# Performance work log

Measured on AMD Instinct MI355X. Metric: run time of the kernel, lower is better.

The kernel has to match this reference:

```python
import jax, jax.numpy as jnp
import numpy as np

N = 500000
EMB = 256
CONT = {0: [0, 1, 4, 6, 7, 8, 9, 10, 11, 12, 13],
        1: [0, 1, 4, 5, 6, 7, 8, 9, 10, 11, 12, 13],
        2: [1, 2, 4, 5, 6, 7, 8, 9, 10, 11, 12, 13],
        3: [2, 3, 4, 5, 6, 7, 8, 9, 10, 11, 12, 13]}
DISC = {0: [2, 3, 5], 1: [2, 3], 2: [0], 3: [0, 1]}
DIMS = {0: {2: 96, 3: 8, 5: 2}, 1: {2: 4, 3: 22}, 2: {0: 6}, 3: {0: 15, 1: 96}}


def _splits(n):
    # emb_dim split across n discrete features, remainder to the first ones
    per, r = EMB // n, EMB % n
    return [per + (1 if i < r else 0) for i in range(n)]


def setup_inputs() -> dict:
    key = jax.random.key(0)
    x = jax.random.normal(jax.random.fold_in(key, 0), (N, 14), jnp.float32)
    # discrete columns must hold valid integer codes for every node type using them
    col_max = {0: 6, 1: 96, 2: 4, 3: 8, 5: 2}
    for c, m in col_max.items():
        v = jax.random.randint(jax.random.fold_in(key, 100 + c), (N,), 0, m)
        x = x.at[:, c].set(v.astype(jnp.float32))
    node_types = jax.random.randint(jax.random.fold_in(key, 1), (N,), 0, 4)
    inp = {"x": x, "node_types": node_types}
    for t in range(4):
        fan_in = len(CONT[t])
        s = float(np.sqrt(6.0 / (fan_in + EMB)))  # xavier_uniform bound
        inp[f"W{t}"] = jax.random.uniform(jax.random.fold_in(key, 10 + t), (EMB, fan_in), jnp.float32, -s, s)
        inp[f"b{t}"] = jax.random.uniform(jax.random.fold_in(key, 20 + t), (EMB,), jnp.float32, -0.05, 0.05)
        dims = _splits(len(DISC[t]))
        for i, c in enumerate(DISC[t]):
            vocab = DIMS[t][c]
            se = float(np.sqrt(6.0 / (vocab + dims[i])))
            inp[f"E{t}_{c}"] = jax.random.uniform(jax.random.fold_in(key, 1000 + 10 * t + c), (vocab, dims[i]), jnp.float32, -se, se)
    return inp


def _forward(x, node_types, Ws, bs, Es):
    out = jnp.zeros((x.shape[0], EMB), x.dtype)
    for t in range(4):  # fixed small set of node types (static MoE dispatch)
        mask = node_types == t  # [N]
        # discrete embeddings: gather per feature column, concat to [N, EMB]
        disc = jnp.concatenate(
            [Es[t][i][x[:, c].astype(jnp.int32)] for i, c in enumerate(DISC[t])], axis=1)
        # continuous projection: [N, in_dim] @ [in_dim, EMB] + bias
        cont = x[:, jnp.array(CONT[t])] @ Ws[t].T + bs[t]
        out = jnp.where(mask[:, None], disc + cont, out)
    return out


def reference(x, node_types, W0, b0, W1, b1, W2, b2, W3, b3,
              E0_2, E0_3, E0_5, E1_2, E1_3, E2_0, E3_0, E3_1):
    Ws = [W0, W1, W2, W3]
    bs = [b0, b1, b2, b3]
    Es = {0: [E0_2, E0_3, E0_5], 1: [E1_2, E1_3], 2: [E2_0], 3: [E3_0, E3_1]}
    return _forward(x, node_types, Ws, bs, Es)
```

## Files before the change

### kernel.cpp

```cpp
#include <hip/hip_runtime.h>

typedef float fvec4 __attribute__((ext_vector_type(4)));

#define NBLK 256
#define TPB  1024
#define NG   16
#define CN   512

#define LAUNDER_PTR(p) asm volatile("" : "+v"(p))

#define O_E0_2 0
#define O_E0_3 8450
#define O_E0_5 9155
#define O_E1_2 9332
#define O_E1_3 9844
#define O_E2_0 12660
#define O_E3_0 14196
#define O_E3_1 16116
#define NTAB   28404
#define XSH    NTAB
#define IDX    (XSH + CN * 16)
#define CNTO   (IDX + 4 * CN)
#define SMEM_FLOATS (CNTO + 4)
#define SMEM_BYTES  (SMEM_FLOATS * 4)

extern __shared__ float smem[];

#define FMA4(K, XV)                                   \
    acc.x = fmaf(w[0][K], (XV), acc.x);               \
    acc.y = fmaf(w[1][K], (XV), acc.y);               \
    acc.z = fmaf(w[2][K], (XV), acc.z);               \
    acc.w = fmaf(w[3][K], (XV), acc.w);

__global__ __launch_bounds__(TPB, 1)
void node_enc_kernel(const float* __restrict__ x,
                     const int* __restrict__ node_types,
                     const float* __restrict__ W0, const float* __restrict__ b0,
                     const float* __restrict__ E0_2, const float* __restrict__ E0_3,
                     const float* __restrict__ E0_5,
                     const float* __restrict__ W1, const float* __restrict__ b1,
                     const float* __restrict__ E1_2, const float* __restrict__ E1_3,
                     const float* __restrict__ W2, const float* __restrict__ b2,
                     const float* __restrict__ E2_0,
                     const float* __restrict__ W3, const float* __restrict__ b3,
                     const float* __restrict__ E3_0, const float* __restrict__ E3_1,
                     float* __restrict__ out, int n_nodes)
{
    const int tid = threadIdx.x;
    const int q   = tid & 63;
    const int h   = tid >> 6;

    auto copy_tab = [&](const float* __restrict__ src, int dst, int n) {
        if ((((uintptr_t)src) & 15) == 0) {
            const int nv = n >> 2;
            for (int i = tid; i < nv; i += TPB) {
                const fvec4 v = *(reinterpret_cast<const fvec4*>(src) + i);
                *reinterpret_cast<fvec4*>(&smem[dst + (i << 2)]) = v;
            }
            for (int i = (nv << 2) + tid; i < n; i += TPB) smem[dst + i] = src[i];
        } else {
            for (int i = tid; i < n; i += TPB) smem[dst + i] = src[i];
        }
    };
    auto copy_tab_pad = [&](const float* __restrict__ src, int dst, int rows, int cols) {
        const int n = rows * cols;
        for (int i = tid; i < n; i += TPB) {
            const int r = i / cols, c2 = i - r * cols;
            smem[dst + r * 88 + c2] = src[i];
        }
    };
    copy_tab_pad(E0_2, O_E0_2, 96, 86);
    copy_tab_pad(E0_3, O_E0_3, 8, 85);
    copy_tab_pad(E0_5, O_E0_5, 2, 85);
    copy_tab(E1_2, O_E1_2, 512);
    copy_tab(E1_3, O_E1_3, 2816);
    copy_tab(E2_0, O_E2_0, 1536);
    copy_tab(E3_0, O_E3_0, 1920);
    copy_tab(E3_1, O_E3_1, 12288);

    const int nch = (n_nodes + CN - 1) / CN;
    const int c0  = (int)(((long long)blockIdx.x * nch) / NBLK);
    const int c1  = (int)(((long long)(blockIdx.x + 1) * nch) / NBLK);

    int* const idx_m = reinterpret_cast<int*>(&smem[IDX]);
    int* const cnt_m = reinterpret_cast<int*>(&smem[CNTO]);
    const int* idx_ro = idx_m;
    const int* cnt_ro = cnt_m;

    auto stage_issue = [&](int c, fvec4& r0, fvec4& r1,
                           float& rs, int& ty, int& nv, int& total, int& cnn) {
        const long long cb = (long long)c * CN;
        cnn   = min(CN, (int)(n_nodes - cb));
        total = cnn * 14;
        nv    = total >> 2;
        const fvec4* vsrc = reinterpret_cast<const fvec4*>(x + cb * 14);
        if (tid < nv)          r0 = __builtin_nontemporal_load(vsrc + tid);
        if (tid + TPB < nv)    r1 = __builtin_nontemporal_load(vsrc + tid + TPB);
        const int sf = (nv << 2) + tid;
        if (sf < total) rs = x[cb * 14 + sf];
        if (tid < cnn)  ty = node_types[cb + tid];
    };
    auto stage_write = [&](const fvec4& r0, const fvec4& r1,
                           float rs, int nv, int total) {
        auto wr1 = [&](int i, const fvec4& v) {
            const int f = i << 2;
            int node = f / 14, col = f - node * 14;
            #pragma unroll
            for (int j = 0; j < 4; ++j) {
                smem[XSH + node * 16 + col] = v[j];
                if (++col == 14) { col = 0; ++node; }
            }
        };
        if (tid < nv)        wr1(tid, r0);
        if (tid + TPB < nv)  wr1(tid + TPB, r1);
        const int sf = (nv << 2) + tid;
        if (sf < total) { const int node = sf / 14, col = sf - node * 14; smem[XSH + node * 16 + col] = rs; }
    };

    auto do_chunk = [&](int c) {
        const long long cb = (long long)c * CN;

        {
            const int m = cnt_ro[0];
            const float* Wp = W0; LAUNDER_PTR(Wp);
            const float* bp = b0; LAUNDER_PTR(bp);
            float w[4][11];
            #pragma unroll
            for (int j = 0; j < 4; ++j) {
                #pragma unroll
                for (int k = 0; k < 11; ++k) w[j][k] = Wp[(4 * q + j) * 11 + k];
            }
            float4 bias;
            bias.x = bp[4 * q]; bias.y = bp[4 * q + 1];
            bias.z = bp[4 * q + 2]; bias.w = bp[4 * q + 3];
            int scv, ebase;
            const bool fb = (q == 21) || (q == 42);
            if (q <= 21)      { scv = 2; ebase = O_E0_2 + 4 * q; }
            else if (q <= 42) { scv = 3; ebase = (O_E0_3 - 86) + 4 * q; }
            else              { scv = 5; ebase = (O_E0_5 - 171) + 4 * q; }
            for (int g = h; g < m; g += NG) {
                const int nl = idx_ro[0 * CN + g];
                const float* xr = &smem[XSH + nl * 16];
                const float4 ra = *reinterpret_cast<const float4*>(xr);
                const float4 rb = *reinterpret_cast<const float4*>(xr + 4);
                const float4 rc = *reinterpret_cast<const float4*>(xr + 8);
                const float2 rd = *reinterpret_cast<const float2*>(xr + 12);
                float4 acc = bias;
                FMA4(0,  ra.x) FMA4(1,  ra.y) FMA4(2,  rb.x) FMA4(3,  rb.z)
                FMA4(4,  rb.w) FMA4(5,  rc.x) FMA4(6,  rc.y) FMA4(7,  rc.z)
                FMA4(8,  rc.w) FMA4(9,  rd.x) FMA4(10, rd.y)
                float4 ev;
                if (fb) {
                    if (q == 21) {
                        const int c2 = (int)xr[2], c3 = (int)xr[3];
                        ev.x = smem[O_E0_2 + c2 * 88 + 84];
                        ev.y = smem[O_E0_2 + c2 * 88 + 85];
                        ev.z = smem[O_E0_3 + c3 * 88 + 0];
                        ev.w = smem[O_E0_3 + c3 * 88 + 1];
                    } else {
                        const int c3 = (int)xr[3], c5 = (int)xr[5];
                        ev.x = smem[O_E0_3 + c3 * 88 + 82];
                        ev.y = smem[O_E0_3 + c3 * 88 + 83];
                        ev.z = smem[O_E0_3 + c3 * 88 + 84];
                        ev.w = smem[O_E0_5 + c5 * 88 + 0];
                    }
                } else {
                    const int code = (int)xr[scv];
                    ev = *reinterpret_cast<const float4*>(&smem[ebase + code * 88]);
                }
                acc.x += ev.x; acc.y += ev.y; acc.z += ev.z; acc.w += ev.w;
                *reinterpret_cast<float4*>(&out[(cb + nl) * 256 + 4 * q]) = acc;
            }
        }

        {
            const int m = cnt_ro[1];
            const float* Wp = W1; LAUNDER_PTR(Wp);
            const float* bp = b1; LAUNDER_PTR(bp);
            float w[4][12];
            #pragma unroll
            for (int j = 0; j < 4; ++j) {
                #pragma unroll
                for (int k = 0; k < 12; ++k) w[j][k] = Wp[(4 * q + j) * 12 + k];
            }
            float4 bias;
            bias.x = bp[4 * q]; bias.y = bp[4 * q + 1];
            bias.z = bp[4 * q + 2]; bias.w = bp[4 * q + 3];
            const int scv   = (q < 32) ? 2 : 3;
            const int ebase = ((q < 32) ? O_E1_2 : (O_E1_3 - 128)) + 4 * q;
            for (int g = h; g < m; g += NG) {
                const int nl = idx_ro[1 * CN + g];
                const float* xr = &smem[XSH + nl * 16];
                const float4 ra = *reinterpret_cast<const float4*>(xr);
                const float4 rb = *reinterpret_cast<const float4*>(xr + 4);
                const float4 rc = *reinterpret_cast<const float4*>(xr + 8);
                const float2 rd = *reinterpret_cast<const float2*>(xr + 12);
                float4 acc = bias;
                FMA4(0,  ra.x) FMA4(1,  ra.y) FMA4(2,  rb.x) FMA4(3,  rb.y)
                FMA4(4,  rb.z) FMA4(5,  rb.w) FMA4(6,  rc.x) FMA4(7,  rc.y)
                FMA4(8,  rc.z) FMA4(9,  rc.w) FMA4(10, rd.x) FMA4(11, rd.y)
                const int code = (int)xr[scv];
                const float4 ev = *reinterpret_cast<const float4*>(&smem[ebase + code * 128]);
                acc.x += ev.x; acc.y += ev.y; acc.z += ev.z; acc.w += ev.w;
                *reinterpret_cast<float4*>(&out[(cb + nl) * 256 + 4 * q]) = acc;
            }
        }

        {
            const int m = cnt_ro[2];
            const float* Wp = W2; LAUNDER_PTR(Wp);
            const float* bp = b2; LAUNDER_PTR(bp);
            float w[4][12];
            #pragma unroll
            for (int j = 0; j < 4; ++j) {
                #pragma unroll
                for (int k = 0; k < 12; ++k) w[j][k] = Wp[(4 * q + j) * 12 + k];
            }
            float4 bias;
            bias.x = bp[4 * q]; bias.y = bp[4 * q + 1];
            bias.z = bp[4 * q + 2]; bias.w = bp[4 * q + 3];
            const int ebase = O_E2_0 + 4 * q;
            for (int g = h; g < m; g += NG) {
                const int nl = idx_ro[2 * CN + g];
                const float* xr = &smem[XSH + nl * 16];
                const float4 ra = *reinterpret_cast<const float4*>(xr);
                const float4 rb = *reinterpret_cast<const float4*>(xr + 4);
                const float4 rc = *reinterpret_cast<const float4*>(xr + 8);
                const float2 rd = *reinterpret_cast<const float2*>(xr + 12);
                float4 acc = bias;
                FMA4(0,  ra.y) FMA4(1,  ra.z) FMA4(2,  rb.x) FMA4(3,  rb.y)
                FMA4(4,  rb.z) FMA4(5,  rb.w) FMA4(6,  rc.x) FMA4(7,  rc.y)
                FMA4(8,  rc.z) FMA4(9,  rc.w) FMA4(10, rd.x) FMA4(11, rd.y)
                const int code = (int)xr[0];
                const float4 ev = *reinterpret_cast<const float4*>(&smem[ebase + code * 256]);
                acc.x += ev.x; acc.y += ev.y; acc.z += ev.z; acc.w += ev.w;
                *reinterpret_cast<float4*>(&out[(cb + nl) * 256 + 4 * q]) = acc;
            }
        }

        {
            const int m = cnt_ro[3];
            const float* Wp = W3; LAUNDER_PTR(Wp);
            const float* bp = b3; LAUNDER_PTR(bp);
            float w[4][12];
            #pragma unroll
            for (int j = 0; j < 4; ++j) {
                #pragma unroll
                for (int k = 0; k < 12; ++k) w[j][k] = Wp[(4 * q + j) * 12 + k];
            }
            float4 bias;
            bias.x = bp[4 * q]; bias.y = bp[4 * q + 1];
            bias.z = bp[4 * q + 2]; bias.w = bp[4 * q + 3];
            const int scv   = (q < 32) ? 0 : 1;
            const int ebase = ((q < 32) ? O_E3_0 : (O_E3_1 - 128)) + 4 * q;
            for (int g = h; g < m; g += NG) {
                const int nl = idx_ro[3 * CN + g];
                const float* xr = &smem[XSH + nl * 16];
                const float4 ra = *reinterpret_cast<const float4*>(xr);
                const float4 rb = *reinterpret_cast<const float4*>(xr + 4);
                const float4 rc = *reinterpret_cast<const float4*>(xr + 8);
                const float2 rd = *reinterpret_cast<const float2*>(xr + 12);
                float4 acc = bias;
                FMA4(0,  ra.z) FMA4(1,  ra.w) FMA4(2,  rb.x) FMA4(3,  rb.y)
                FMA4(4,  rb.z) FMA4(5,  rb.w) FMA4(6,  rc.x) FMA4(7,  rc.y)
                FMA4(8,  rc.z) FMA4(9,  rc.w) FMA4(10, rd.x) FMA4(11, rd.y)
                const int code = (int)xr[scv];
                const float4 ev = *reinterpret_cast<const float4*>(&smem[ebase + code * 128]);
                acc.x += ev.x; acc.y += ev.y; acc.z += ev.z; acc.w += ev.w;
                *reinterpret_cast<float4*>(&out[(cb + nl) * 256 + 4 * q]) = acc;
            }
        }
    };

    {
        fvec4 r0, r1; float rs = 0.f; int ty = 0, nv = 0, total = 0, cnn = 0;
        if (c0 < c1) {
            stage_issue(c0, r0, r1, rs, ty, nv, total, cnn);
            stage_write(r0, r1, rs, nv, total);
            if (tid < 4) cnt_m[tid] = 0;
        }
        __syncthreads();
        if (c0 < c1 && tid < cnn) {
            const int p = atomicAdd(&cnt_m[ty], 1);
            idx_m[ty * CN + p] = tid;
        }
        __syncthreads();
    }

    for (int c = c0; c < c1; ++c) {
        fvec4 r0, r1; float rs = 0.f; int ty = 0, nv = 0, total = 0, cnn = 0;
        const bool hasnext = (c + 1 < c1);
        if (hasnext) stage_issue(c + 1, r0, r1, rs, ty, nv, total, cnn);
        do_chunk(c);
        __syncthreads();
        if (hasnext) {
            stage_write(r0, r1, rs, nv, total);
            if (tid < 4) cnt_m[tid] = 0;
        }
        __syncthreads();
        if (hasnext && tid < cnn) {
            const int p = atomicAdd(&cnt_m[ty], 1);
            idx_m[ty * CN + p] = tid;
        }
        __syncthreads();
    }
}

extern "C" void kernel_launch(void* const* d_in, const int* in_sizes, int n_in,
                              void* d_out, int out_size, void* d_ws, size_t ws_size,
                              hipStream_t stream) {
    const float* xp   = (const float*)d_in[0];
    const int*   ntp  = (const int*)d_in[1];
    const float* W0 = (const float*)d_in[2];
    const float* b0 = (const float*)d_in[3];
    const float* E0_2 = (const float*)d_in[4];
    const float* E0_3 = (const float*)d_in[5];
    const float* E0_5 = (const float*)d_in[6];
    const float* W1 = (const float*)d_in[7];
    const float* b1 = (const float*)d_in[8];
    const float* E1_2 = (const float*)d_in[9];
    const float* E1_3 = (const float*)d_in[10];
    const float* W2 = (const float*)d_in[11];
    const float* b2 = (const float*)d_in[12];
    const float* E2_0 = (const float*)d_in[13];
    const float* W3 = (const float*)d_in[14];
    const float* b3 = (const float*)d_in[15];
    const float* E3_0 = (const float*)d_in[16];
    const float* E3_1 = (const float*)d_in[17];
    float* outp = (float*)d_out;

    const int n_nodes = in_sizes[1];

    (void)hipFuncSetAttribute(reinterpret_cast<const void*>(node_enc_kernel),
                              hipFuncAttributeMaxDynamicSharedMemorySize, SMEM_BYTES);

    node_enc_kernel<<<NBLK, TPB, SMEM_BYTES, stream>>>(
        xp, ntp, W0, b0, E0_2, E0_3, E0_5, W1, b1, E1_2, E1_3,
        W2, b2, E2_0, W3, b3, E3_0, E3_1, outp, n_nodes);
}
```

Baseline: 127.4 us.

## Stage weights and bias in LDS and store embedding tables as bf16

Each block now copies all four weight matrices, transposed, plus the biases into shared memory. Each per-type section loads its weights as float4 from LDS, where it used to make scalar global loads on every chunk. The embedding tables are converted to bf16 when copied into LDS, which halves their footprint and the per-lookup LDS traffic, and they are expanded back to fp32 with shifts. This lowers the precision of the embedding values, which could break exact-match tolerance, and it makes the per-block prologue longer.

New measurement: 135.5 us. 1.06x slower.

```diff
diff --git a/kernel.cpp b/kernel.cpp
--- a/kernel.cpp
+++ b/kernel.cpp
@@ -1,13 +1,25 @@
 #include <hip/hip_runtime.h>
+#include <hip/hip_bf16.h>
 
 typedef float fvec4 __attribute__((ext_vector_type(4)));
+typedef unsigned short ushort_t;
+typedef unsigned int uint_t;
 
 #define NBLK 256
 #define TPB  1024
 #define NG   16
 #define CN   512
 
-#define LAUNDER_PTR(p) asm volatile("" : "+v"(p))
+#define WT0    0
+#define WT1    2816
+#define WT2    5888
+#define WT3    8960
+#define BIASF  12032
+#define XSHF   13056
+#define IDXI   21248
+#define CNTI   23296
+#define SMEM_FLOATS 23300
+#define TABU   46600
 
 #define O_E0_2 0
 #define O_E0_3 8450
@@ -17,20 +29,24 @@
 #define O_E2_0 12660
 #define O_E3_0 14196
 #define O_E3_1 16116
-#define NTAB   28404
-#define XSH    NTAB
-#define IDX    (XSH + CN * 16)
-#define CNTO   (IDX + 4 * CN)
-#define SMEM_FLOATS (CNTO + 4)
-#define SMEM_BYTES  (SMEM_FLOATS * 4)
+#define NTABU  28404
+#define SMEM_BYTES (93200 + NTABU * 2)
 
 extern __shared__ float smem[];
 
+__device__ __forceinline__ ushort_t f2bf(float v) {
+    __hip_bfloat16 h = __float2bfloat16(v);
+    return *reinterpret_cast<ushort_t*>(&h);
+}
+__device__ __forceinline__ float bf2f(ushort_t u) {
+    return __uint_as_float(((uint_t)u) << 16);
+}
+
 #define FMA4(K, XV)                                   \
-    acc.x = fmaf(w[0][K], (XV), acc.x);               \
-    acc.y = fmaf(w[1][K], (XV), acc.y);               \
-    acc.z = fmaf(w[2][K], (XV), acc.z);               \
-    acc.w = fmaf(w[3][K], (XV), acc.w);
+    acc.x = fmaf(w4[K].x, (XV), acc.x);               \
+    acc.y = fmaf(w4[K].y, (XV), acc.y);               \
+    acc.z = fmaf(w4[K].z, (XV), acc.z);               \
+    acc.w = fmaf(w4[K].w, (XV), acc.w);
 
 __global__ __launch_bounds__(TPB, 1)
 void node_enc_kernel(const float* __restrict__ x,
@@ -50,40 +66,47 @@
     const int q   = tid & 63;
     const int h   = tid >> 6;
 
-    auto copy_tab = [&](const float* __restrict__ src, int dst, int n) {
-        if ((((uintptr_t)src) & 15) == 0) {
-            const int nv = n >> 2;
-            for (int i = tid; i < nv; i += TPB) {
-                const fvec4 v = *(reinterpret_cast<const fvec4*>(src) + i);
-                *reinterpret_cast<fvec4*>(&smem[dst + (i << 2)]) = v;
-            }
-            for (int i = (nv << 2) + tid; i < n; i += TPB) smem[dst + i] = src[i];
-        } else {
-            for (int i = tid; i < n; i += TPB) smem[dst + i] = src[i];
-        }
-    };
-    auto copy_tab_pad = [&](const float* __restrict__ src, int dst, int rows, int cols) {
+    ushort_t* const tab = reinterpret_cast<ushort_t*>(smem) + TABU;
+
+    auto copy_wt = [&](const float* __restrict__ W, const float* __restrict__ b,
+                       int wt, int t, int NW) {
+        const int n = 256 * NW;
+        for (int i = tid; i < n; i += TPB) {
+            const int col = i / NW, k = i - col * NW;
+            smem[wt + k * 256 + col] = W[i];
+        }
+        for (int i = tid; i < 256; i += TPB) smem[BIASF + t * 256 + i] = b[i];
+    };
+    copy_wt(W0, b0, WT0, 0, 11);
+    copy_wt(W1, b1, WT1, 1, 12);
+    copy_wt(W2, b2, WT2, 2, 12);
+    copy_wt(W3, b3, WT3, 3, 12);
+
+    auto copy_tab_bf = [&](const float* __restrict__ src, int dst, int n) {
+        for (int i = tid; i < n; i += TPB) tab[dst + i] = f2bf(src[i]);
+    };
+    auto copy_tab_pad_bf = [&](const float* __restrict__ src, int dst, int rows, int cols) {
         const int n = rows * cols;
         for (int i = tid; i < n; i += TPB) {
             const int r = i / cols, c2 = i - r * cols;
-            smem[dst + r * 88 + c2] = src[i];
-        }
-    };
-    copy_tab_pad(E0_2, O_E0_2, 96, 86);
-    copy_tab_pad(E0_3, O_E0_3, 8, 85);
-    copy_tab_pad(E0_5, O_E0_5, 2, 85);
-    copy_tab(E1_2, O_E1_2, 512);
-    copy_tab(E1_3, O_E1_3, 2816);
-    copy_tab(E2_0, O_E2_0, 1536);
-    copy_tab(E3_0, O_E3_0, 1920);
-    copy_tab(E3_1, O_E3_1, 12288);
+            tab[dst + r * 88 + c2] = f2bf(src[i]);
+        }
+    };
+    copy_tab_pad_bf(E0_2, O_E0_2, 96, 86);
+    copy_tab_pad_bf(E0_3, O_E0_3, 8, 85);
+    copy_tab_pad_bf(E0_5, O_E0_5, 2, 85);
+    copy_tab_bf(E1_2, O_E1_2, 512);
+    copy_tab_bf(E1_3, O_E1_3, 2816);
+    copy_tab_bf(E2_0, O_E2_0, 1536);
+    copy_tab_bf(E3_0, O_E3_0, 1920);
+    copy_tab_bf(E3_1, O_E3_1, 12288);
 
     const int nch = (n_nodes + CN - 1) / CN;
     const int c0  = (int)(((long long)blockIdx.x * nch) / NBLK);
     const int c1  = (int)(((long long)(blockIdx.x + 1) * nch) / NBLK);
 
-    int* const idx_m = reinterpret_cast<int*>(&smem[IDX]);
-    int* const cnt_m = reinterpret_cast<int*>(&smem[CNTO]);
+    int* const idx_m = reinterpret_cast<int*>(&smem[IDXI]);
+    int* const cnt_m = reinterpret_cast<int*>(&smem[CNTI]);
     const int* idx_ro = idx_m;
     const int* cnt_ro = cnt_m;
 
@@ -107,14 +130,14 @@
             int node = f / 14, col = f - node * 14;
             #pragma unroll
             for (int j = 0; j < 4; ++j) {
-                smem[XSH + node * 16 + col] = v[j];
+                smem[XSHF + node * 16 + col] = v[j];
                 if (++col == 14) { col = 0; ++node; }
             }
         };
         if (tid < nv)        wr1(tid, r0);
         if (tid + TPB < nv)  wr1(tid + TPB, r1);
         const int sf = (nv << 2) + tid;
-        if (sf < total) { const int node = sf / 14, col = sf - node * 14; smem[XSH + node * 16 + col] = rs; }
+        if (sf < total) { const int node = sf / 14, col = sf - node * 14; smem[XSHF + node * 16 + col] = rs; }
     };
 
     auto do_chunk = [&](int c) {
@@ -122,17 +145,11 @@
 
         {
             const int m = cnt_ro[0];
-            const float* Wp = W0; LAUNDER_PTR(Wp);
-            const float* bp = b0; LAUNDER_PTR(bp);
-            float w[4][11];
-            #pragma unroll
-            for (int j = 0; j < 4; ++j) {
-                #pragma unroll
-                for (int k = 0; k < 11; ++k) w[j][k] = Wp[(4 * q + j) * 11 + k];
-            }
-            float4 bias;
-            bias.x = bp[4 * q]; bias.y = bp[4 * q + 1];
-            bias.z = bp[4 * q + 2]; bias.w = bp[4 * q + 3];
+            float4 w4[11];
+            #pragma unroll
+            for (int k = 0; k < 11; ++k)
+                w4[k] = *reinterpret_cast<const float4*>(&smem[WT0 + k * 256 + 4 * q]);
+            const float4 bias = *reinterpret_cast<const float4*>(&smem[BIASF + 0 * 256 + 4 * q]);
             int scv, ebase;
             const bool fb = (q == 21) || (q == 42);
             if (q <= 21)      { scv = 2; ebase = O_E0_2 + 4 * q; }
@@ -140,7 +157,7 @@
             else              { scv = 5; ebase = (O_E0_5 - 171) + 4 * q; }
             for (int g = h; g < m; g += NG) {
                 const int nl = idx_ro[0 * CN + g];
-                const float* xr = &smem[XSH + nl * 16];
+                const float* xr = &smem[XSHF + nl * 16];
                 const float4 ra = *reinterpret_cast<const float4*>(xr);
                 const float4 rb = *reinterpret_cast<const float4*>(xr + 4);
                 const float4 rc = *reinterpret_cast<const float4*>(xr + 8);
@@ -153,20 +170,24 @@
                 if (fb) {
                     if (q == 21) {
                         const int c2 = (int)xr[2], c3 = (int)xr[3];
-                        ev.x = smem[O_E0_2 + c2 * 88 + 84];
-                        ev.y = smem[O_E0_2 + c2 * 88 + 85];
-                        ev.z = smem[O_E0_3 + c3 * 88 + 0];
-                        ev.w = smem[O_E0_3 + c3 * 88 + 1];
+                        ev.x = bf2f(tab[O_E0_2 + c2 * 88 + 84]);
+                        ev.y = bf2f(tab[O_E0_2 + c2 * 88 + 85]);
+                        ev.z = bf2f(tab[O_E0_3 + c3 * 88 + 0]);
+                        ev.w = bf2f(tab[O_E0_3 + c3 * 88 + 1]);
                     } else {
                         const int c3 = (int)xr[3], c5 = (int)xr[5];
-                        ev.x = smem[O_E0_3 + c3 * 88 + 82];
-                        ev.y = smem[O_E0_3 + c3 * 88 + 83];
-                        ev.z = smem[O_E0_3 + c3 * 88 + 84];
-                        ev.w = smem[O_E0_5 + c5 * 88 + 0];
+                        ev.x = bf2f(tab[O_E0_3 + c3 * 88 + 82]);
+                        ev.y = bf2f(tab[O_E0_3 + c3 * 88 + 83]);
+                        ev.z = bf2f(tab[O_E0_3 + c3 * 88 + 84]);
+                        ev.w = bf2f(tab[O_E0_5 + c5 * 88 + 0]);
                     }
                 } else {
                     const int code = (int)xr[scv];
-                    ev = *reinterpret_cast<const float4*>(&smem[ebase + code * 88]);
+                    const uint2 u = *reinterpret_cast<const uint2*>(&tab[ebase + code * 88]);
+                    ev.x = __uint_as_float(u.x << 16);
+                    ev.y = __uint_as_float(u.x & 0xffff0000u);
+                    ev.z = __uint_as_float(u.y << 16);
+                    ev.w = __uint_as_float(u.y & 0xffff0000u);
                 }
                 acc.x += ev.x; acc.y += ev.y; acc.z += ev.z; acc.w += ev.w;
                 *reinterpret_cast<float4*>(&out[(cb + nl) * 256 + 4 * q]) = acc;
@@ -175,22 +196,16 @@
 
         {
             const int m = cnt_ro[1];
-            const float* Wp = W1; LAUNDER_PTR(Wp);
-            const float* bp = b1; LAUNDER_PTR(bp);
-            float w[4][12];
-            #pragma unroll
-            for (int j = 0; j < 4; ++j) {
-                #pragma unroll
-                for (int k = 0; k < 12; ++k) w[j][k] = Wp[(4 * q + j) * 12 + k];
-            }
-            float4 bias;
-            bias.x = bp[4 * q]; bias.y = bp[4 * q + 1];
-            bias.z = bp[4 * q + 2]; bias.w = bp[4 * q + 3];
+            float4 w4[12];
+            #pragma unroll
+            for (int k = 0; k < 12; ++k)
+                w4[k] = *reinterpret_cast<const float4*>(&smem[WT1 + k * 256 + 4 * q]);
+            const float4 bias = *reinterpret_cast<const float4*>(&smem[BIASF + 1 * 256 + 4 * q]);
             const int scv   = (q < 32) ? 2 : 3;
             const int ebase = ((q < 32) ? O_E1_2 : (O_E1_3 - 128)) + 4 * q;
             for (int g = h; g < m; g += NG) {
                 const int nl = idx_ro[1 * CN + g];
-                const float* xr = &smem[XSH + nl * 16];
+                const float* xr = &smem[XSHF + nl * 16];
                 const float4 ra = *reinterpret_cast<const float4*>(xr);
                 const float4 rb = *reinterpret_cast<const float4*>(xr + 4);
                 const float4 rc = *reinterpret_cast<const float4*>(xr + 8);
@@ -200,7 +215,12 @@
                 FMA4(4,  rb.z) FMA4(5,  rb.w) FMA4(6,  rc.x) FMA4(7,  rc.y)
                 FMA4(8,  rc.z) FMA4(9,  rc.w) FMA4(10, rd.x) FMA4(11, rd.y)
                 const int code = (int)xr[scv];
-                const float4 ev = *reinterpret_cast<const float4*>(&smem[ebase + code * 128]);
+                const uint2 u = *reinterpret_cast<const uint2*>(&tab[ebase + code * 128]);
+                float4 ev;
+                ev.x = __uint_as_float(u.x << 16);
+                ev.y = __uint_as_float(u.x & 0xffff0000u);
+                ev.z = __uint_as_float(u.y << 16);
+                ev.w = __uint_as_float(u.y & 0xffff0000u);
                 acc.x += ev.x; acc.y += ev.y; acc.z += ev.z; acc.w += ev.w;
                 *reinterpret_cast<float4*>(&out[(cb + nl) * 256 + 4 * q]) = acc;
             }
@@ -208,21 +228,15 @@
 
         {
             const int m = cnt_ro[2];
-            const float* Wp = W2; LAUNDER_PTR(Wp);
-            const float* bp = b2; LAUNDER_PTR(bp);
-            float w[4][12];
-            #pragma unroll
-            for (int j = 0; j < 4; ++j) {
-                #pragma unroll
-                for (int k = 0; k < 12; ++k) w[j][k] = Wp[(4 * q + j) * 12 + k];
-            }
-            float4 bias;
-            bias.x = bp[4 * q]; bias.y = bp[4 * q + 1];
-            bias.z = bp[4 * q + 2]; bias.w = bp[4 * q + 3];
+            float4 w4[12];
+            #pragma unroll
+            for (int k = 0; k < 12; ++k)
+                w4[k] = *reinterpret_cast<const float4*>(&smem[WT2 + k * 256 + 4 * q]);
+            const float4 bias = *reinterpret_cast<const float4*>(&smem[BIASF + 2 * 256 + 4 * q]);
             const int ebase = O_E2_0 + 4 * q;
             for (int g = h; g < m; g += NG) {
                 const int nl = idx_ro[2 * CN + g];
-                const float* xr = &smem[XSH + nl * 16];
+                const float* xr = &smem[XSHF + nl * 16];
                 const float4 ra = *reinterpret_cast<const float4*>(xr);
                 const float4 rb = *reinterpret_cast<const float4*>(xr + 4);
                 const float4 rc = *reinterpret_cast<const float4*>(xr + 8);
@@ -232,7 +246,12 @@
                 FMA4(4,  rb.z) FMA4(5,  rb.w) FMA4(6,  rc.x) FMA4(7,  rc.y)
                 FMA4(8,  rc.z) FMA4(9,  rc.w) FMA4(10, rd.x) FMA4(11, rd.y)
                 const int code = (int)xr[0];
-                const float4 ev = *reinterpret_cast<const float4*>(&smem[ebase + code * 256]);
+                const uint2 u = *reinterpret_cast<const uint2*>(&tab[ebase + code * 256]);
+                float4 ev;
+                ev.x = __uint_as_float(u.x << 16);
+                ev.y = __uint_as_float(u.x & 0xffff0000u);
+                ev.z = __uint_as_float(u.y << 16);
+                ev.w = __uint_as_float(u.y & 0xffff0000u);
                 acc.x += ev.x; acc.y += ev.y; acc.z += ev.z; acc.w += ev.w;
                 *reinterpret_cast<float4*>(&out[(cb + nl) * 256 + 4 * q]) = acc;
             }
@@ -240,22 +259,16 @@
 
         {
             const int m = cnt_ro[3];
-            const float* Wp = W3; LAUNDER_PTR(Wp);
-            const float* bp = b3; LAUNDER_PTR(bp);
-            float w[4][12];
-            #pragma unroll
-            for (int j = 0; j < 4; ++j) {
-                #pragma unroll
-                for (int k = 0; k < 12; ++k) w[j][k] = Wp[(4 * q + j) * 12 + k];
-            }
-            float4 bias;
-            bias.x = bp[4 * q]; bias.y = bp[4 * q + 1];
-            bias.z = bp[4 * q + 2]; bias.w = bp[4 * q + 3];
+            float4 w4[12];
+            #pragma unroll
+            for (int k = 0; k < 12; ++k)
+                w4[k] = *reinterpret_cast<const float4*>(&smem[WT3 + k * 256 + 4 * q]);
+            const float4 bias = *reinterpret_cast<const float4*>(&smem[BIASF + 3 * 256 + 4 * q]);
             const int scv   = (q < 32) ? 0 : 1;
             const int ebase = ((q < 32) ? O_E3_0 : (O_E3_1 - 128)) + 4 * q;
             for (int g = h; g < m; g += NG) {
                 const int nl = idx_ro[3 * CN + g];
-                const float* xr = &smem[XSH + nl * 16];
+                const float* xr = &smem[XSHF + nl * 16];
                 const float4 ra = *reinterpret_cast<const float4*>(xr);
                 const float4 rb = *reinterpret_cast<const float4*>(xr + 4);
                 const float4 rc = *reinterpret_cast<const float4*>(xr + 8);
@@ -265,7 +278,12 @@
                 FMA4(4,  rb.z) FMA4(5,  rb.w) FMA4(6,  rc.x) FMA4(7,  rc.y)
                 FMA4(8,  rc.z) FMA4(9,  rc.w) FMA4(10, rd.x) FMA4(11, rd.y)
                 const int code = (int)xr[scv];
-                const float4 ev = *reinterpret_cast<const float4*>(&smem[ebase + code * 128]);
+                const uint2 u = *reinterpret_cast<const uint2*>(&tab[ebase + code * 128]);
+                float4 ev;
+                ev.x = __uint_as_float(u.x << 16);
+                ev.y = __uint_as_float(u.x & 0xffff0000u);
+                ev.z = __uint_as_float(u.y << 16);
+                ev.w = __uint_as_float(u.y & 0xffff0000u);
                 acc.x += ev.x; acc.y += ev.y; acc.z += ev.z; acc.w += ev.w;
                 *reinterpret_cast<float4*>(&out[(cb + nl) * 256 + 4 * q]) = acc;
             }
```
